# Kernel tuning notes

Measured on AMD Instinct MI355X. Metric: run time of the kernel, lower is better.

Reference implementation:

```python
import jax, jax.numpy as jnp
import numpy as np

COMMITMENT_BETA = 0.25


def setup_inputs() -> dict:
    key = jax.random.key(0)
    k1, k2, k3 = jax.random.split(key, 3)
    Q, N, K, D = 4096, 50000, 1024, 256
    return {
        "query_emb": jax.random.normal(k1, (Q, D), dtype=jnp.float32),
        "entity_emb": jax.random.normal(k2, (N, D), dtype=jnp.float32),
        "codebook": jax.random.normal(k3, (K, D), dtype=jnp.float32),
    }


def reference(query_emb, entity_emb, codebook):
    x = entity_emb  # [N, D]
    # squared distance == argmin of torch.norm distance; avoids [N,K,D] tensor)
    x2 = jnp.sum(x * x, axis=1, keepdims=True)          # [N, 1]
    c2 = jnp.sum(codebook * codebook, axis=1)           # [K]
    d2 = x2 + c2[None, :] - 2.0 * (x @ codebook.T)      # [N, K]
    nearest_idx = jnp.argmin(d2, axis=1)                # [N]
    quantized = codebook[nearest_idx]                   # [N, D]

    sg = jax.lax.stop_gradient
    vq_loss = jnp.mean((sg(quantized) - x) ** 2) + COMMITMENT_BETA * jnp.mean(
        (quantized - sg(x)) ** 2
    )
    score = query_emb @ quantized.T                     # [Q, N]
    return score, vq_loss, nearest_idx
```

## Files before the change

kernel.cpp:

```cpp
#include <hip/hip_runtime.h>

#define QDIM 4096
#define NDIM 50000
#define KDIM 1024
#define DDIM 256
#define NBLK 782
#define TAU  0.3f

typedef _Float16 half8 __attribute__((ext_vector_type(8)));
typedef float    f32x4 __attribute__((ext_vector_type(4)));

#define GLD16(srcp, dstp)                                                              \
    __builtin_amdgcn_global_load_lds((const __attribute__((address_space(1))) void*)(srcp), \
                                     (__attribute__((address_space(3))) void*)(dstp), 16, 0, 0)

__device__ float np_pairwise_sq(const float* a) {
#pragma clang fp contract(off)
    float res[2];
    for (int h = 0; h < 2; ++h) {
        const float* p = a + h * 128;
        float r0 = p[0] * p[0], r1 = p[1] * p[1], r2 = p[2] * p[2], r3 = p[3] * p[3];
        float r4 = p[4] * p[4], r5 = p[5] * p[5], r6 = p[6] * p[6], r7 = p[7] * p[7];
        for (int i = 8; i < 128; i += 8) {
            r0 += p[i + 0] * p[i + 0];
            r1 += p[i + 1] * p[i + 1];
            r2 += p[i + 2] * p[i + 2];
            r3 += p[i + 3] * p[i + 3];
            r4 += p[i + 4] * p[i + 4];
            r5 += p[i + 5] * p[i + 5];
            r6 += p[i + 6] * p[i + 6];
            r7 += p[i + 7] * p[i + 7];
        }
        res[h] = ((r0 + r1) + (r2 + r3)) + ((r4 + r5) + (r6 + r7));
    }
    return res[0] + res[1];
}

__device__ float np_exact_d2(const float* __restrict__ xr, const float* __restrict__ cp,
                             float x2, float c2v) {
    float dot = 0.f;
    for (int d = 0; d < DDIM; ++d) dot = __builtin_fmaf(cp[d], xr[d], dot);
    return (x2 + c2v) - 2.0f * dot;
}

__global__ __launch_bounds__(256) void prep_kernel(const float* __restrict__ cb,
                                                   float* __restrict__ c2np,
                                                   int* __restrict__ refCtr) {
    int k = blockIdx.x * 256 + threadIdx.x;
    if (k < KDIM) c2np[k] = np_pairwise_sq(cb + (size_t)k * DDIM);
    if (k < 2) refCtr[k] = 0;
}

__global__ __launch_bounds__(64) void cvt_kernel(const float* __restrict__ cb,
                                                 _Float16* __restrict__ cbh) {
    int k = blockIdx.x;
    int t = threadIdx.x;
    const float* src = cb + (size_t)k * DDIM + t * 4;
    _Float16* dst = cbh + (size_t)k * DDIM + t * 4;
    float4 v = *(const float4*)src;
    dst[0] = (_Float16)v.x; dst[1] = (_Float16)v.y;
    dst[2] = (_Float16)v.z; dst[3] = (_Float16)v.w;
}


__global__ __launch_bounds__(256) void argmin16_kernel(const float* __restrict__ E,
                                                       const _Float16* __restrict__ CBH,
                                                       const float* __restrict__ c2,
                                                       int* __restrict__ idxOut,
                                                       float* __restrict__ idxF,
                                                       float* __restrict__ lossPart,
                                                       int* __restrict__ refCtr,
                                                       int4* __restrict__ refQuad,
                                                       int* __restrict__ refFull) {
    __shared__ _Float16 Buf[64 * 256];
    __shared__ float xsq[64];
    __shared__ float rowd2s[64];
    int tid = threadIdx.x;
    int lane = tid & 63;
    int w = tid >> 6;
    int rowBase = blockIdx.x * 64;

    {
        int r = tid >> 2, seg = tid & 3;
        int rg = rowBase + r; if (rg >= NDIM) rg = NDIM - 1;
        const float* src = E + (size_t)rg * DDIM + seg * 64;
        float x2p = 0.f;
#pragma unroll
        for (int i = 0; i < 8; ++i) {
            float4 v0 = *(const float4*)&src[i * 8];
            float4 v1 = *(const float4*)&src[i * 8 + 4];
            x2p += v0.x * v0.x + v0.y * v0.y + v0.z * v0.z + v0.w * v0.w;
            x2p += v1.x * v1.x + v1.y * v1.y + v1.z * v1.z + v1.w * v1.w;
            half8 h;
            h[0] = (_Float16)v0.x; h[1] = (_Float16)v0.y; h[2] = (_Float16)v0.z; h[3] = (_Float16)v0.w;
            h[4] = (_Float16)v1.x; h[5] = (_Float16)v1.y; h[6] = (_Float16)v1.z; h[7] = (_Float16)v1.w;
            int slot = (seg * 8 + i) ^ (r & 7);
            *(half8*)&Buf[r * 256 + slot * 8] = h;
        }
        x2p += __shfl_down(x2p, 2, 4);
        x2p += __shfl_down(x2p, 1, 4);
        if (seg == 0) xsq[r] = x2p;
    }
    __syncthreads();

    half8 a[8];
    {
        int rA = w * 16 + (lane & 15);
        int g = lane >> 4;
#pragma unroll
        for (int s8 = 0; s8 < 8; ++s8) {
            int slot = (s8 * 4 + g) ^ (rA & 7);
            a[s8] = *(half8*)&Buf[rA * 256 + slot * 8];
        }
    }

    const _Float16* bsrc[8];
    _Float16* bdst[8];
    {
        int rowLoc = lane >> 5;
        int chunk = lane & 31;
#pragma unroll
        for (int i = 0; i < 8; ++i) {
            int row = w * 16 + i * 2 + rowLoc;
            int sc = chunk ^ (row & 7);
            bsrc[i] = CBH + (size_t)row * DDIM + sc * 8;
            bdst[i] = &Buf[(w * 16 + i * 2) * 256];
        }
    }

    float m1[4] = {1e30f, 1e30f, 1e30f, 1e30f};
    float m2[4] = {1e30f, 1e30f, 1e30f, 1e30f};
    float m3[4] = {1e30f, 1e30f, 1e30f, 1e30f};
    int   i1[4] = {0, 0, 0, 0};
    int   i2[4] = {0, 0, 0, 0};

    for (int kc = 0; kc < 16; ++kc) {
        __syncthreads();
        size_t koff = (size_t)kc * 64 * DDIM;
#pragma unroll
        for (int i = 0; i < 8; ++i) GLD16(bsrc[i] + koff, bdst[i]);
        float cc[4];
#pragma unroll
        for (int t = 0; t < 4; ++t) cc[t] = c2[kc * 64 + t * 16 + (lane & 15)];
        __syncthreads();

        int g = lane >> 4;
#pragma unroll
        for (int t = 0; t < 4; ++t) {
            f32x4 acc = {0.f, 0.f, 0.f, 0.f};
            int cB = t * 16 + (lane & 15);
#pragma unroll
            for (int s8 = 0; s8 < 8; ++s8) {
                int slot = (s8 * 4 + g) ^ (cB & 7);
                half8 b = *(half8*)&Buf[cB * 256 + slot * 8];
                acc = __builtin_amdgcn_mfma_f32_16x16x32_f16(a[s8], b, acc, 0, 0, 0);
            }
            int ki = kc * 64 + cB;
#pragma unroll
            for (int j = 0; j < 4; ++j) {
                float v = cc[t] - 2.0f * acc[j];
                if (v < m1[j])      { m3[j] = m2[j]; m2[j] = m1[j]; i2[j] = i1[j]; m1[j] = v; i1[j] = ki; }
                else if (v < m2[j]) { m3[j] = m2[j]; m2[j] = v; i2[j] = ki; }
                else if (v < m3[j]) { m3[j] = v; }
            }
        }
    }
#pragma unroll
    for (int j = 0; j < 4; ++j) {
        for (int m = 8; m >= 1; m >>= 1) {
            float o1 = __shfl_xor(m1[j], m, 16);
            int   oi1 = __shfl_xor(i1[j], m, 16);
            float o2 = __shfl_xor(m2[j], m, 16);
            int   oi2 = __shfl_xor(i2[j], m, 16);
            float o3 = __shfl_xor(m3[j], m, 16);
            float a1, a2, a3, b1, b2, b3; int ai1, ai2, bi1, bi2;
            if (o1 < m1[j] || (o1 == m1[j] && oi1 < i1[j])) {
                a1 = o1; ai1 = oi1; a2 = o2; ai2 = oi2; a3 = o3;
                b1 = m1[j]; bi1 = i1[j]; b2 = m2[j]; bi2 = i2[j]; b3 = m3[j];
            } else {
                a1 = m1[j]; ai1 = i1[j]; a2 = m2[j]; ai2 = i2[j]; a3 = m3[j];
                b1 = o1; bi1 = oi1; b2 = o2; bi2 = oi2; b3 = o3;
            }
            (void)bi2; (void)b3;
            m1[j] = a1; i1[j] = ai1;
            if (b1 < a2 || (b1 == a2 && bi1 < ai2)) {
                m2[j] = b1; i2[j] = bi1; m3[j] = fminf(a2, b2);
            } else {
                m2[j] = a2; i2[j] = ai2; m3[j] = fminf(a3, b1);
            }
        }
    }
    if ((lane & 15) == 0) {
#pragma unroll
        for (int j = 0; j < 4; ++j) {
            int rloc = w * 16 + (lane >> 4) * 4 + j;
            int row = rowBase + rloc;
            if (row < NDIM) {
                idxOut[row] = i1[j];
                idxF[row] = (float)i1[j];
                rowd2s[rloc] = xsq[rloc] + m1[j];
                if (m2[j] - m1[j] < TAU) {
                    int p = atomicAdd(&refCtr[0], 1);
                    if ((unsigned)p < (unsigned)NDIM) {
                        int4 q; q.x = row; q.y = i1[j]; q.z = i2[j]; q.w = 0;
                        refQuad[p] = q;
                    }
                }
                if (m3[j] - m1[j] < TAU) {
                    int p = atomicAdd(&refCtr[1], 1);
                    if ((unsigned)p < (unsigned)NDIM) refFull[p] = row;
                }
            } else {
                rowd2s[rloc] = 0.f;
            }
        }
    }
    __syncthreads();
    if (tid == 0) {
        float s = 0.f;
        for (int i = 0; i < 64; ++i) s += rowd2s[i];
        lossPart[blockIdx.x] = s;
    }
}

__global__ __launch_bounds__(256) void sgemm16_kernel(const float* __restrict__ Q,
                                                      const _Float16* __restrict__ CBH,
                                                      float* __restrict__ S) {
    __shared__ _Float16 Buf[64 * 256];
    int tid = threadIdx.x;
    int lane = tid & 63;
    int w = tid >> 6;
    int rowBase = blockIdx.x * 64;
    int kcBase = blockIdx.y * 2;

    {
        int r = tid >> 2, seg = tid & 3;
        const float* src = Q + (size_t)(rowBase + r) * DDIM + seg * 64;
#pragma unroll
        for (int i = 0; i < 8; ++i) {
            float4 v0 = *(const float4*)&src[i * 8];
            float4 v1 = *(const float4*)&src[i * 8 + 4];
            half8 h;
            h[0] = (_Float16)v0.x; h[1] = (_Float16)v0.y; h[2] = (_Float16)v0.z; h[3] = (_Float16)v0.w;
            h[4] = (_Float16)v1.x; h[5] = (_Float16)v1.y; h[6] = (_Float16)v1.z; h[7] = (_Float16)v1.w;
            int slot = (seg * 8 + i) ^ (r & 7);
            *(half8*)&Buf[r * 256 + slot * 8] = h;
        }
    }
    __syncthreads();
    half8 a[8];
    {
        int rA = w * 16 + (lane & 15);
        int g = lane >> 4;
#pragma unroll
        for (int s8 = 0; s8 < 8; ++s8) {
            int slot = (s8 * 4 + g) ^ (rA & 7);
            a[s8] = *(half8*)&Buf[rA * 256 + slot * 8];
        }
    }

    const _Float16* bsrc[8];
    _Float16* bdst[8];
    {
        int rowLoc = lane >> 5;
        int chunk = lane & 31;
#pragma unroll
        for (int i = 0; i < 8; ++i) {
            int row = w * 16 + i * 2 + rowLoc;
            int sc = chunk ^ (row & 7);
            bsrc[i] = CBH + (size_t)row * DDIM + sc * 8;
            bdst[i] = &Buf[(w * 16 + i * 2) * 256];
        }
    }

    for (int kci = 0; kci < 2; ++kci) {
        int kc = kcBase + kci;
        __syncthreads();
        size_t koff = (size_t)kc * 64 * DDIM;
#pragma unroll
        for (int i = 0; i < 8; ++i) GLD16(bsrc[i] + koff, bdst[i]);
        __syncthreads();

        int g = lane >> 4;
#pragma unroll
        for (int t = 0; t < 4; ++t) {
            f32x4 acc = {0.f, 0.f, 0.f, 0.f};
            int cB = t * 16 + (lane & 15);
#pragma unroll
            for (int s8 = 0; s8 < 8; ++s8) {
                int slot = (s8 * 4 + g) ^ (cB & 7);
                half8 b = *(half8*)&Buf[cB * 256 + slot * 8];
                acc = __builtin_amdgcn_mfma_f32_16x16x32_f16(a[s8], b, acc, 0, 0, 0);
            }
#pragma unroll
            for (int j = 0; j < 4; ++j) {
                int row = rowBase + w * 16 + g * 4 + j;
                S[(size_t)row * KDIM + kc * 64 + cB] = acc[j];
            }
        }
    }
}

__global__ __launch_bounds__(256) void refcand_kernel(const float* __restrict__ E,
                                                      const float* __restrict__ CB,
                                                      const float* __restrict__ c2np,
                                                      const int* __restrict__ refCtr,
                                                      const int4* __restrict__ refQuad,
                                                      int* __restrict__ idxOut,
                                                      float* __restrict__ idxF) {
    int i = blockIdx.x * 256 + threadIdx.x;
    int count = refCtr[0];
    if (count > NDIM) count = NDIM;
    if (i >= count) return;
    int4 q = refQuad[i];
    int row = q.x, a = q.y, b = q.z;
    const float* xr = E + (size_t)row * DDIM;
    float x2 = np_pairwise_sq(xr);
    float va = np_exact_d2(xr, CB + (size_t)a * DDIM, x2, c2np[a]);
    float vb = np_exact_d2(xr, CB + (size_t)b * DDIM, x2, c2np[b]);
    int win = (vb < va || (vb == va && b < a)) ? b : a;
    idxOut[row] = win;
    idxF[row] = (float)win;
}

__global__ __launch_bounds__(256) void refine_kernel(const float* __restrict__ E,
                                                     const float* __restrict__ CB,
                                                     const float* __restrict__ c2np,
                                                     const int* __restrict__ refCtr,
                                                     const int* __restrict__ refFull,
                                                     int* __restrict__ idxOut,
                                                     float* __restrict__ idxF) {
    __shared__ float xrow[DDIM];
    __shared__ float x2sh;
    __shared__ float wval[4];
    __shared__ int widx[4];
    int tid = threadIdx.x;
    int count = refCtr[1];
    if (count > NDIM) count = NDIM;
    for (int b = blockIdx.x; b < count; b += gridDim.x) {
        int row = refFull[b];
        xrow[tid] = E[(size_t)row * DDIM + tid];
        __syncthreads();
        if (tid == 0) x2sh = np_pairwise_sq(xrow);
        __syncthreads();
        float best = 1e30f;
        int bidx = 0x7fffffff;
#pragma unroll
        for (int kk = 0; kk < 4; ++kk) {
            int k = tid + kk * 256;
            const float* cp = CB + (size_t)k * DDIM;
            float dot = 0.f;
            for (int d = 0; d < DDIM; ++d) dot = __builtin_fmaf(cp[d], xrow[d], dot);
            float t1 = x2sh + c2np[k];
            float v = t1 - 2.0f * dot;
            if (v < best || (v == best && k < bidx)) { best = v; bidx = k; }
        }
        for (int m = 32; m >= 1; m >>= 1) {
            float ov = __shfl_xor(best, m, 64);
            int   oi = __shfl_xor(bidx, m, 64);
            if (ov < best || (ov == best && oi < bidx)) { best = ov; bidx = oi; }
        }
        if ((tid & 63) == 0) { wval[tid >> 6] = best; widx[tid >> 6] = bidx; }
        __syncthreads();
        if (tid == 0) {
            float bv = wval[0]; int bi = widx[0];
#pragma unroll
            for (int w = 1; w < 4; ++w)
                if (wval[w] < bv || (wval[w] == bv && widx[w] < bi)) { bv = wval[w]; bi = widx[w]; }
            idxOut[row] = bi;
            idxF[row] = (float)bi;
        }
        __syncthreads();
    }
}

__global__ void loss_kernel(const float* __restrict__ lossPart, float* __restrict__ out) {
    int t = threadIdx.x;
    float s = 0.f;
    for (int i = t; i < NBLK; i += 64) s += lossPart[i];
    for (int m = 32; m >= 1; m >>= 1) s += __shfl_down(s, m, 64);
    if (t == 0) out[0] = 1.25f * s / (float)(NDIM * DDIM);
}

__global__ __launch_bounds__(256) void gather_kernel(const float* __restrict__ S,
                                                     const int* __restrict__ idx,
                                                     float* __restrict__ score) {
    __shared__ float Srow[4 * 1024];
    int tid = threadIdx.x;
    int qBase = blockIdx.y * 4;
    int nBase = blockIdx.x * 2048;
#pragma unroll
    for (int i = 0; i < 4; ++i) {
        int o = (tid + i * 256) * 4;
        *(float4*)&Srow[o] = *(const float4*)&S[(size_t)qBase * KDIM + o];
    }
    __syncthreads();
#pragma unroll
    for (int s = 0; s < 2; ++s) {
        int n = nBase + s * 1024 + tid * 4;
        if (n < NDIM) {
            int4 id = *(const int4*)&idx[n];
#pragma unroll
            for (int q = 0; q < 4; ++q) {
                const float* sp = &Srow[q * 1024];
                f32x4 v = {sp[id.x], sp[id.y], sp[id.z], sp[id.w]};
                __builtin_nontemporal_store(v, (f32x4*)&score[(size_t)(qBase + q) * NDIM + n]);
            }
        }
    }
}

extern "C" void kernel_launch(void* const* d_in, const int* in_sizes, int n_in,
                              void* d_out, int out_size, void* d_ws, size_t ws_size,
                              hipStream_t stream) {
    const float* query  = (const float*)d_in[0];
    const float* entity = (const float*)d_in[1];
    const float* cb     = (const float*)d_in[2];
    float* out = (float*)d_out;
    char* ws = (char*)d_ws;

    float*     S        = (float*)ws;
    float*     c2np     = (float*)(ws + 16777216);
    int*       idxW     = (int*)  (ws + 16781312);
    int*       refCtr   = (int*)  (ws + 16981312);
    int4*      refQuad  = (int4*) (ws + 16981376);
    int*       refFull  = (int*)  (ws + 17781376);
    float*     lossPart = (float*)(ws + 17981376);
    _Float16*  cbh      = (_Float16*)(ws + 17984512);

    size_t QN = (size_t)QDIM * NDIM;
    float* score   = out;
    float* lossOut = out + QN;
    float* idxF    = out + QN + 1;

    prep_kernel<<<dim3(4), dim3(256), 0, stream>>>(cb, c2np, refCtr);
    cvt_kernel<<<dim3(KDIM), dim3(64), 0, stream>>>(cb, cbh);
    sgemm16_kernel<<<dim3(QDIM / 64, 8), dim3(256), 0, stream>>>(query, cbh, S);
    argmin16_kernel<<<dim3(NBLK), dim3(256), 0, stream>>>(entity, cbh, c2np, idxW, idxF,
                                                          lossPart, refCtr, refQuad, refFull);
    refcand_kernel<<<dim3((NDIM + 255) / 256), dim3(256), 0, stream>>>(entity, cb, c2np, refCtr,
                                                                       refQuad, idxW, idxF);
    refine_kernel<<<dim3(256), dim3(256), 0, stream>>>(entity, cb, c2np, refCtr, refFull, idxW, idxF);
    loss_kernel<<<dim3(1), dim3(64), 0, stream>>>(lossPart, lossOut);
    gather_kernel<<<dim3((NDIM + 2047) / 2048, QDIM / 4), dim3(256), 0, stream>>>(S, idxW, score);
}
```

Before: 372.9 us.

## Double argmin rows per block, load A directly to registers, parallelize c2 prep

The argmin kernel now covers 128 entity rows per block, with each wave handling two 16-row tiles. Every codebook chunk staged in LDS is therefore reused across twice as many MFMA ops, and the block count is halved. Entity rows are loaded straight into MFMA A-fragment registers instead of going through LDS, which removes a barrier and the LDS round trip. The codebook-norm prep kernel spreads each code across 16 lanes using shuffles, with a changed summation order. The trade-offs are higher register pressure, fewer blocks for occupancy, and possible bitwise differences in c2 that could alter which candidates the refine pass picks up.

New measurement: 343.2 us. -8.0%, faster.

```diff
diff --git a/kernel.cpp b/kernel.cpp
--- a/kernel.cpp
+++ b/kernel.cpp
@@ -4,7 +4,7 @@
 #define NDIM 50000
 #define KDIM 1024
 #define DDIM 256
-#define NBLK 782
+#define ABLK 391
 #define TAU  0.3f
 
 typedef _Float16 half8 __attribute__((ext_vector_type(8)));
@@ -46,9 +46,21 @@
 __global__ __launch_bounds__(256) void prep_kernel(const float* __restrict__ cb,
                                                    float* __restrict__ c2np,
                                                    int* __restrict__ refCtr) {
-    int k = blockIdx.x * 256 + threadIdx.x;
-    if (k < KDIM) c2np[k] = np_pairwise_sq(cb + (size_t)k * DDIM);
-    if (k < 2) refCtr[k] = 0;
+#pragma clang fp contract(off)
+    int tid = threadIdx.x;
+    int code = blockIdx.x * 16 + (tid >> 4);
+    int l = tid & 15;
+    int h = l >> 3, j = l & 7;
+    const float* p = cb + (size_t)code * DDIM + h * 128;
+    float v0 = p[j];
+    float r = v0 * v0;
+    for (int i = 8; i < 128; i += 8) { float v = p[i + j]; r = r + v * v; }
+    r += __shfl_xor(r, 1, 16);
+    r += __shfl_xor(r, 2, 16);
+    r += __shfl_xor(r, 4, 16);
+    r += __shfl_xor(r, 8, 16);
+    if (l == 0) c2np[code] = r;
+    if (code == 0 && l == 0) { refCtr[0] = 0; refCtr[1] = 0; }
 }
 
 __global__ __launch_bounds__(64) void cvt_kernel(const float* __restrict__ cb,
@@ -62,56 +74,45 @@
     dst[2] = (_Float16)v.z; dst[3] = (_Float16)v.w;
 }
 
-
-__global__ __launch_bounds__(256) void argmin16_kernel(const float* __restrict__ E,
-                                                       const _Float16* __restrict__ CBH,
-                                                       const float* __restrict__ c2,
-                                                       int* __restrict__ idxOut,
-                                                       float* __restrict__ idxF,
-                                                       float* __restrict__ lossPart,
-                                                       int* __restrict__ refCtr,
-                                                       int4* __restrict__ refQuad,
-                                                       int* __restrict__ refFull) {
+__global__ __launch_bounds__(256) void argmin128_kernel(const float* __restrict__ E,
+                                                        const _Float16* __restrict__ CBH,
+                                                        const float* __restrict__ c2,
+                                                        int* __restrict__ idxOut,
+                                                        float* __restrict__ idxF,
+                                                        float* __restrict__ lossPart,
+                                                        int* __restrict__ refCtr,
+                                                        int4* __restrict__ refQuad,
+                                                        int* __restrict__ refFull) {
     __shared__ _Float16 Buf[64 * 256];
-    __shared__ float xsq[64];
-    __shared__ float rowd2s[64];
+    __shared__ float xsq[128];
+    __shared__ float rowd2s[128];
     int tid = threadIdx.x;
     int lane = tid & 63;
     int w = tid >> 6;
-    int rowBase = blockIdx.x * 64;
-
-    {
-        int r = tid >> 2, seg = tid & 3;
-        int rg = rowBase + r; if (rg >= NDIM) rg = NDIM - 1;
-        const float* src = E + (size_t)rg * DDIM + seg * 64;
-        float x2p = 0.f;
-#pragma unroll
-        for (int i = 0; i < 8; ++i) {
-            float4 v0 = *(const float4*)&src[i * 8];
-            float4 v1 = *(const float4*)&src[i * 8 + 4];
-            x2p += v0.x * v0.x + v0.y * v0.y + v0.z * v0.z + v0.w * v0.w;
-            x2p += v1.x * v1.x + v1.y * v1.y + v1.z * v1.z + v1.w * v1.w;
+    int g = lane >> 4, cl = lane & 15;
+    int rowBase = blockIdx.x * 128 + w * 32;
+
+    half8 a[2][8];
+#pragma unroll
+    for (int rt = 0; rt < 2; ++rt) {
+        int row = rowBase + rt * 16 + cl;
+        int rg = row < NDIM ? row : NDIM - 1;
+        const float* src = E + (size_t)rg * DDIM + g * 8;
+        float s = 0.f;
+#pragma unroll
+        for (int s8 = 0; s8 < 8; ++s8) {
+            float4 v0 = *(const float4*)&src[s8 * 32];
+            float4 v1 = *(const float4*)&src[s8 * 32 + 4];
+            s += v0.x * v0.x + v0.y * v0.y + v0.z * v0.z + v0.w * v0.w;
+            s += v1.x * v1.x + v1.y * v1.y + v1.z * v1.z + v1.w * v1.w;
             half8 h;
             h[0] = (_Float16)v0.x; h[1] = (_Float16)v0.y; h[2] = (_Float16)v0.z; h[3] = (_Float16)v0.w;
             h[4] = (_Float16)v1.x; h[5] = (_Float16)v1.y; h[6] = (_Float16)v1.z; h[7] = (_Float16)v1.w;
-            int slot = (seg * 8 + i) ^ (r & 7);
-            *(half8*)&Buf[r * 256 + slot * 8] = h;
-        }
-        x2p += __shfl_down(x2p, 2, 4);
-        x2p += __shfl_down(x2p, 1, 4);
-        if (seg == 0) xsq[r] = x2p;
-    }
-    __syncthreads();
-
-    half8 a[8];
-    {
-        int rA = w * 16 + (lane & 15);
-        int g = lane >> 4;
-#pragma unroll
-        for (int s8 = 0; s8 < 8; ++s8) {
-            int slot = (s8 * 4 + g) ^ (rA & 7);
-            a[s8] = *(half8*)&Buf[rA * 256 + slot * 8];
-        }
+            a[rt][s8] = h;
+        }
+        s += __shfl_xor(s, 16, 64);
+        s += __shfl_xor(s, 32, 64);
+        if (g == 0) xsq[w * 32 + rt * 16 + cl] = s;
     }
 
     const _Float16* bsrc[8];
@@ -128,11 +129,11 @@
         }
     }
 
-    float m1[4] = {1e30f, 1e30f, 1e30f, 1e30f};
-    float m2[4] = {1e30f, 1e30f, 1e30f, 1e30f};
-    float m3[4] = {1e30f, 1e30f, 1e30f, 1e30f};
-    int   i1[4] = {0, 0, 0, 0};
-    int   i2[4] = {0, 0, 0, 0};
+    float m1[2][4] = {{1e30f, 1e30f, 1e30f, 1e30f}, {1e30f, 1e30f, 1e30f, 1e30f}};
+    float m2[2][4] = {{1e30f, 1e30f, 1e30f, 1e30f}, {1e30f, 1e30f, 1e30f, 1e30f}};
+    float m3[2][4] = {{1e30f, 1e30f, 1e30f, 1e30f}, {1e30f, 1e30f, 1e30f, 1e30f}};
+    int   i1[2][4] = {{0, 0, 0, 0}, {0, 0, 0, 0}};
+    int   i2[2][4] = {{0, 0, 0, 0}, {0, 0, 0, 0}};
 
     for (int kc = 0; kc < 16; ++kc) {
         __syncthreads();
@@ -141,84 +142,92 @@
         for (int i = 0; i < 8; ++i) GLD16(bsrc[i] + koff, bdst[i]);
         float cc[4];
 #pragma unroll
-        for (int t = 0; t < 4; ++t) cc[t] = c2[kc * 64 + t * 16 + (lane & 15)];
-        __syncthreads();
-
-        int g = lane >> 4;
+        for (int t = 0; t < 4; ++t) cc[t] = c2[kc * 64 + t * 16 + cl];
+        __syncthreads();
+
 #pragma unroll
         for (int t = 0; t < 4; ++t) {
-            f32x4 acc = {0.f, 0.f, 0.f, 0.f};
-            int cB = t * 16 + (lane & 15);
-#pragma unroll
-            for (int s8 = 0; s8 < 8; ++s8) {
-                int slot = (s8 * 4 + g) ^ (cB & 7);
-                half8 b = *(half8*)&Buf[cB * 256 + slot * 8];
-                acc = __builtin_amdgcn_mfma_f32_16x16x32_f16(a[s8], b, acc, 0, 0, 0);
-            }
+            int cB = t * 16 + cl;
             int ki = kc * 64 + cB;
 #pragma unroll
+            for (int rt = 0; rt < 2; ++rt) {
+                f32x4 acc = {0.f, 0.f, 0.f, 0.f};
+#pragma unroll
+                for (int s8 = 0; s8 < 8; ++s8) {
+                    int slot = (s8 * 4 + g) ^ (cB & 7);
+                    half8 b = *(half8*)&Buf[cB * 256 + slot * 8];
+                    acc = __builtin_amdgcn_mfma_f32_16x16x32_f16(a[rt][s8], b, acc, 0, 0, 0);
+                }
+#pragma unroll
+                for (int j = 0; j < 4; ++j) {
+                    float v = cc[t] - 2.0f * acc[j];
+                    if (v < m1[rt][j])      { m3[rt][j] = m2[rt][j]; m2[rt][j] = m1[rt][j]; i2[rt][j] = i1[rt][j]; m1[rt][j] = v; i1[rt][j] = ki; }
+                    else if (v < m2[rt][j]) { m3[rt][j] = m2[rt][j]; m2[rt][j] = v; i2[rt][j] = ki; }
+                    else if (v < m3[rt][j]) { m3[rt][j] = v; }
+                }
+            }
+        }
+    }
+#pragma unroll
+    for (int rt = 0; rt < 2; ++rt) {
+#pragma unroll
+        for (int j = 0; j < 4; ++j) {
+            for (int m = 8; m >= 1; m >>= 1) {
+                float o1 = __shfl_xor(m1[rt][j], m, 16);
+                int   oi1 = __shfl_xor(i1[rt][j], m, 16);
+                float o2 = __shfl_xor(m2[rt][j], m, 16);
+                int   oi2 = __shfl_xor(i2[rt][j], m, 16);
+                float o3 = __shfl_xor(m3[rt][j], m, 16);
+                float a1, a2, a3, b1, b2, b3; int ai1, ai2, bi1, bi2;
+                if (o1 < m1[rt][j] || (o1 == m1[rt][j] && oi1 < i1[rt][j])) {
+                    a1 = o1; ai1 = oi1; a2 = o2; ai2 = oi2; a3 = o3;
+                    b1 = m1[rt][j]; bi1 = i1[rt][j]; b2 = m2[rt][j]; bi2 = i2[rt][j]; b3 = m3[rt][j];
+                } else {
+                    a1 = m1[rt][j]; ai1 = i1[rt][j]; a2 = m2[rt][j]; ai2 = i2[rt][j]; a3 = m3[rt][j];
+                    b1 = o1; bi1 = oi1; b2 = o2; bi2 = oi2; b3 = o3;
+                }
+                (void)bi2; (void)b3;
+                m1[rt][j] = a1; i1[rt][j] = ai1;
+                if (b1 < a2 || (b1 == a2 && bi1 < ai2)) {
+                    m2[rt][j] = b1; i2[rt][j] = bi1; m3[rt][j] = fminf(a2, b2);
+                } else {
+                    m2[rt][j] = a2; i2[rt][j] = ai2; m3[rt][j] = fminf(a3, b1);
+                }
+            }
+        }
+    }
+    if (cl == 0) {
+#pragma unroll
+        for (int rt = 0; rt < 2; ++rt) {
+#pragma unroll
             for (int j = 0; j < 4; ++j) {
-                float v = cc[t] - 2.0f * acc[j];
-                if (v < m1[j])      { m3[j] = m2[j]; m2[j] = m1[j]; i2[j] = i1[j]; m1[j] = v; i1[j] = ki; }
-                else if (v < m2[j]) { m3[j] = m2[j]; m2[j] = v; i2[j] = ki; }
-                else if (v < m3[j]) { m3[j] = v; }
-            }
-        }
-    }
-#pragma unroll
-    for (int j = 0; j < 4; ++j) {
-        for (int m = 8; m >= 1; m >>= 1) {
-            float o1 = __shfl_xor(m1[j], m, 16);
-            int   oi1 = __shfl_xor(i1[j], m, 16);
-            float o2 = __shfl_xor(m2[j], m, 16);
-            int   oi2 = __shfl_xor(i2[j], m, 16);
-            float o3 = __shfl_xor(m3[j], m, 16);
-            float a1, a2, a3, b1, b2, b3; int ai1, ai2, bi1, bi2;
-            if (o1 < m1[j] || (o1 == m1[j] && oi1 < i1[j])) {
-                a1 = o1; ai1 = oi1; a2 = o2; ai2 = oi2; a3 = o3;
-                b1 = m1[j]; bi1 = i1[j]; b2 = m2[j]; bi2 = i2[j]; b3 = m3[j];
-            } else {
-                a1 = m1[j]; ai1 = i1[j]; a2 = m2[j]; ai2 = i2[j]; a3 = m3[j];
-                b1 = o1; bi1 = oi1; b2 = o2; bi2 = oi2; b3 = o3;
-            }
-            (void)bi2; (void)b3;
-            m1[j] = a1; i1[j] = ai1;
-            if (b1 < a2 || (b1 == a2 && bi1 < ai2)) {
-                m2[j] = b1; i2[j] = bi1; m3[j] = fminf(a2, b2);
-            } else {
-                m2[j] = a2; i2[j] = ai2; m3[j] = fminf(a3, b1);
-            }
-        }
-    }
-    if ((lane & 15) == 0) {
-#pragma unroll
-        for (int j = 0; j < 4; ++j) {
-            int rloc = w * 16 + (lane >> 4) * 4 + j;
-            int row = rowBase + rloc;
-            if (row < NDIM) {
-                idxOut[row] = i1[j];
-                idxF[row] = (float)i1[j];
-                rowd2s[rloc] = xsq[rloc] + m1[j];
-                if (m2[j] - m1[j] < TAU) {
-                    int p = atomicAdd(&refCtr[0], 1);
-                    if ((unsigned)p < (unsigned)NDIM) {
-                        int4 q; q.x = row; q.y = i1[j]; q.z = i2[j]; q.w = 0;
-                        refQuad[p] = q;
+                int rloc = w * 32 + rt * 16 + g * 4 + j;
+                int row = blockIdx.x * 128 + rloc;
+                if (row < NDIM) {
+                    idxOut[row] = i1[rt][j];
+                    idxF[row] = (float)i1[rt][j];
+                    rowd2s[rloc] = xsq[rloc] + m1[rt][j];
+                    if (m2[rt][j] - m1[rt][j] < TAU) {
+                        int p = atomicAdd(&refCtr[0], 1);
+                        if ((unsigned)p < (unsigned)NDIM) {
+                            int4 q; q.x = row; q.y = i1[rt][j]; q.z = i2[rt][j]; q.w = 0;
+                            refQuad[p] = q;
+                        }
                     }
+                    if (m3[rt][j] - m1[rt][j] < TAU) {
+                        int p = atomicAdd(&refCtr[1], 1);
+                        if ((unsigned)p < (unsigned)NDIM) refFull[p] = row;
+                    }
+                } else {
+                    rowd2s[rloc] = 0.f;
                 }
-                if (m3[j] - m1[j] < TAU) {
-                    int p = atomicAdd(&refCtr[1], 1);
-                    if ((unsigned)p < (unsigned)NDIM) refFull[p] = row;
-                }
-            } else {
-                rowd2s[rloc] = 0.f;
             }
         }
     }
     __syncthreads();
     if (tid == 0) {
         float s = 0.f;
-        for (int i = 0; i < 64; ++i) s += rowd2s[i];
+        for (int i = 0; i < 128; ++i) s += rowd2s[i];
         lossPart[blockIdx.x] = s;
     }
 }
@@ -377,7 +386,7 @@
 __global__ void loss_kernel(const float* __restrict__ lossPart, float* __restrict__ out) {
     int t = threadIdx.x;
     float s = 0.f;
-    for (int i = t; i < NBLK; i += 64) s += lossPart[i];
+    for (int i = t; i < ABLK; i += 64) s += lossPart[i];
     for (int m = 32; m >= 1; m >>= 1) s += __shfl_down(s, m, 64);
     if (t == 0) out[0] = 1.25f * s / (float)(NDIM * DDIM);
 }
@@ -433,11 +442,11 @@
     float* lossOut = out + QN;
     float* idxF    = out + QN + 1;
 
-    prep_kernel<<<dim3(4), dim3(256), 0, stream>>>(cb, c2np, refCtr);
+    prep_kernel<<<dim3(KDIM / 16), dim3(256), 0, stream>>>(cb, c2np, refCtr);
     cvt_kernel<<<dim3(KDIM), dim3(64), 0, stream>>>(cb, cbh);
     sgemm16_kernel<<<dim3(QDIM / 64, 8), dim3(256), 0, stream>>>(query, cbh, S);
-    argmin16_kernel<<<dim3(NBLK), dim3(256), 0, stream>>>(entity, cbh, c2np, idxW, idxF,
-                                                          lossPart, refCtr, refQuad, refFull);
+    argmin128_kernel<<<dim3(ABLK), dim3(256), 0, stream>>>(entity, cbh, c2np, idxW, idxF,
+                                                           lossPart, refCtr, refQuad, refFull);
     refcand_kernel<<<dim3((NDIM + 255) / 256), dim3(256), 0, stream>>>(entity, cb, c2np, refCtr,
                                                                        refQuad, idxW, idxF);
     refine_kernel<<<dim3(256), dim3(256), 0, stream>>>(entity, cb, c2np, refCtr, refFull, idxW, idxF);
```
